# Kernel optimization log

Measured on AMD Instinct MI355X. Metric: run time of the kernel, lower is better.

Reference implementation:

```python
import jax, jax.numpy as jnp
import numpy as np

N, F_IN, E, DIM, G, C = 50000, 128, 800000, 64, 128, 10
BN_EPS = 1e-5


def setup_inputs() -> dict:
    key = jax.random.key(0)
    ks = jax.random.split(key, 24)
    x = jax.random.normal(ks[0], (N, F_IN), dtype=jnp.float32)
    edge_index = jax.random.randint(ks[1], (2, E), 0, N, dtype=jnp.int32)
    batch = jnp.sort(jax.random.randint(ks[2], (N,), 0, G, dtype=jnp.int32))

    def lin(k, fan_in, shape):
        b = 1.0 / np.sqrt(fan_in)
        return jax.random.uniform(k, shape, jnp.float32, -b, b)

    # layer 1 MLP: [F_IN->DIM], [DIM->DIM]
    W1a, b1a = lin(ks[3], F_IN, (F_IN, DIM)), lin(ks[4], F_IN, (DIM,))
    W1b, b1b = lin(ks[5], DIM, (DIM, DIM)), lin(ks[6], DIM, (DIM,))
    # layers 2-5 MLPs stacked: [4, DIM, DIM]
    Wa = jnp.stack([lin(jax.random.fold_in(ks[7], i), DIM, (DIM, DIM)) for i in range(4)])
    ba = jnp.stack([lin(jax.random.fold_in(ks[8], i), DIM, (DIM,)) for i in range(4)])
    Wb = jnp.stack([lin(jax.random.fold_in(ks[9], i), DIM, (DIM, DIM)) for i in range(4)])
    bb = jnp.stack([lin(jax.random.fold_in(ks[10], i), DIM, (DIM,)) for i in range(4)])
    gammas = jnp.ones((5, DIM), jnp.float32)
    betas = jnp.zeros((5, DIM), jnp.float32)
    fc1_w, fc1_b = lin(ks[11], DIM, (DIM, DIM)), lin(ks[12], DIM, (DIM,))
    fc2_w, fc2_b = lin(ks[13], DIM, (DIM, C)), lin(ks[14], DIM, (C,))
    return dict(x=x, edge_index=edge_index, batch=batch,
                W1a=W1a, b1a=b1a, W1b=W1b, b1b=b1b,
                Wa=Wa, ba=ba, Wb=Wb, bb=bb,
                gammas=gammas, betas=betas,
                fc1_w=fc1_w, fc1_b=fc1_b, fc2_w=fc2_w, fc2_b=fc2_b)


def _gin_conv(x, edge_index, W1, b1, W2, b2):
    # PyG GINConv (eps=0): MLP((1+eps)*x + scatter_add of source feats at targets)
    agg = jax.ops.segment_sum(x[edge_index[0]], edge_index[1], num_segments=N)
    h = x + agg
    h = jnp.maximum(h @ W1 + b1, 0.0) @ W2 + b2
    return h


def _bn(h, gamma, beta):
    # BatchNorm1d, training mode (batch statistics, biased variance)
    mean = h.mean(axis=0)
    var = h.var(axis=0)
    return (h - mean) * jax.lax.rsqrt(var + BN_EPS) * gamma + beta


def reference(x, edge_index, batch, W1a, b1a, W1b, b1b, Wa, ba, Wb, bb,
              gammas, betas, fc1_w, fc1_b, fc2_w, fc2_b):
    h = jnp.maximum(_gin_conv(x, edge_index, W1a, b1a, W1b, b1b), 0.0)
    h = _bn(h, gammas[0], betas[0])
    for i in range(4):
        h = jnp.maximum(_gin_conv(h, edge_index, Wa[i], ba[i], Wb[i], bb[i]), 0.0)
        h = _bn(h, gammas[i + 1], betas[i + 1])
    pooled = jax.ops.segment_sum(h, batch, num_segments=G)  # global_add_pool -> [G, DIM]
    z = jnp.maximum(pooled @ fc1_w + fc1_b, 0.0)
    z = z @ fc2_w + fc2_b
    return jax.nn.log_softmax(z, axis=-1)
```

## Files before the change

kernel.cpp:

```cpp
#include <hip/hip_runtime.h>
#include <hip/hip_fp16.h>


constexpr int N = 50000;
constexpr int E = 800000;
constexpr int G = 128;
constexpr int MAXDEG = 64;
constexpr float BN_EPS = 1e-5f;

__device__ inline float4 ld4(const float* p) { return *(const float4*)p; }
__device__ inline void st4(float* p, float4 v) { *(float4*)p = v; }

union HF2 { __half2 h2[2]; float2 f2; };

__global__ __launch_bounds__(256) void count_fill_kernel(
    const int* __restrict__ ei, int* __restrict__ deg, unsigned short* __restrict__ ell)
{
    int e = blockIdx.x * 256 + threadIdx.x;
    if (e < E) {
        int s = ei[e];
        int d = ei[E + e];
        int slot = atomicAdd(&deg[d], 1);
        if (slot < MAXDEG) ell[d * MAXDEG + slot] = (unsigned short)s;
    }
}

__global__ __launch_bounds__(256) void pad_kernel(
    const int* __restrict__ deg, unsigned short* __restrict__ ell)
{
    int n = blockIdx.x * 256 + threadIdx.x;
    if (n < N) {
        int dgc = min(deg[n], MAXDEG);
        int p = (dgc + 7) & ~7;
        for (int s = dgc; s < p; s++) ell[n * MAXDEG + s] = (unsigned short)N;
    }
}

__global__ __launch_bounds__(256) void xw_kernel(
    const float* __restrict__ x, const float* __restrict__ W, __half* __restrict__ out)
{
    int tid = threadIdx.x;
    int ty = tid >> 4, tx = tid & 15;
    int base = blockIdx.x * 64;

    float acc[4][4];
#pragma unroll
    for (int r = 0; r < 4; r++)
#pragma unroll
        for (int cc = 0; cc < 4; cc++) acc[r][cc] = 0.f;

    int rr[4];
#pragma unroll
    for (int r = 0; r < 4; r++) rr[r] = min(base + 4 * ty + r, N - 1);

#pragma unroll 4
    for (int c = 0; c < 128; c++) {
        float4 w4 = ld4(W + c * 64 + 4 * tx);
#pragma unroll
        for (int r = 0; r < 4; r++) {
            float a = x[(size_t)rr[r] * 128 + c];
            acc[r][0] += a * w4.x; acc[r][1] += a * w4.y;
            acc[r][2] += a * w4.z; acc[r][3] += a * w4.w;
        }
    }
#pragma unroll
    for (int r = 0; r < 4; r++) {
        int node = base + 4 * ty + r;
        if (node < N) {
            HF2 u;
            u.h2[0] = __floats2half2_rn(acc[r][0], acc[r][1]);
            u.h2[1] = __floats2half2_rn(acc[r][2], acc[r][3]);
            *(float2*)(out + (size_t)node * 64 + 4 * tx) = u.f2;
        }
    }
}

__global__ __launch_bounds__(64) void reduce_stats_kernel(
    const float* __restrict__ partials, float* __restrict__ stats, int nb)
{
    int c = blockIdx.x;
    int lane = threadIdx.x;
    float s = 0.f;
    for (int i = lane; i < nb; i += 64)
        s += partials[(size_t)i * 128 + c];
#pragma unroll
    for (int off = 32; off > 0; off >>= 1)
        s += __shfl_down(s, off, 64);
    if (lane == 0) stats[c] = s;
}

template <bool FIRST>
__global__ __launch_bounds__(256) void layer_kernel(
    const __half* __restrict__ hin, const unsigned short* __restrict__ ell,
    const int* __restrict__ deg,
    const float* __restrict__ statsPrev, const float* __restrict__ gamma, const float* __restrict__ beta,
    const float* __restrict__ bias0,
    const float* __restrict__ W1, const float* __restrict__ b1,
    const float* __restrict__ W2, const float* __restrict__ b2,
    __half* __restrict__ hout, float* __restrict__ statsPart)
{
    __shared__ float sV[64 * 68];
    __shared__ float sStat[128];

    int tid = threadIdx.x, lane = tid & 63, wv = tid >> 6;
    if (tid < 128) sStat[tid] = 0.f;

    int base = blockIdx.x * 64;
    int n8 = lane >> 3, f = lane & 7;

    float sc[8], sh[8], b0[8];
    if constexpr (FIRST) {
#pragma unroll
        for (int q = 0; q < 2; q++) {
            float4 b4 = ld4(bias0 + 8 * f + 4 * q);
            b0[4 * q + 0] = b4.x; b0[4 * q + 1] = b4.y;
            b0[4 * q + 2] = b4.z; b0[4 * q + 3] = b4.w;
        }
    } else {
#pragma unroll
        for (int q = 0; q < 2; q++) {
            float4 s1 = ld4(statsPrev + 8 * f + 4 * q);
            float4 s2 = ld4(statsPrev + 64 + 8 * f + 4 * q);
            float4 g4 = ld4(gamma + 8 * f + 4 * q);
            float4 be4 = ld4(beta + 8 * f + 4 * q);
            float m[4] = { s1.x / N, s1.y / N, s1.z / N, s1.w / N };
            float v2[4] = { s2.x / N, s2.y / N, s2.z / N, s2.w / N };
            float gg[4] = { g4.x, g4.y, g4.z, g4.w };
            float bb4[4] = { be4.x, be4.y, be4.z, be4.w };
#pragma unroll
            for (int i = 0; i < 4; i++) {
                float s = gg[i] * rsqrtf(v2[i] - m[i] * m[i] + BN_EPS);
                sc[4 * q + i] = s;
                sh[4 * q + i] = bb4[i] - m[i] * s;
            }
        }
    }

#pragma unroll
    for (int kk = 0; kk < 2; kk++) {
        int node = base + wv * 16 + kk * 8 + n8;
        int nd = (node < N) ? node : N;
        int dg = (node < N) ? deg[node] : 0;
        int dgc = min(dg, MAXDEG);
        int p = (dgc + 7) & ~7;
        const unsigned short* row = ell + (size_t)nd * MAXDEG;

        __half2 ap[8][4];
#pragma unroll
        for (int r = 0; r < 8; r++)
#pragma unroll
            for (int k = 0; k < 4; k++) ap[r][k] = __half2(__float2half(0.f), __float2half(0.f));

        float4 rown = ld4((const float*)(hin + (size_t)nd * 64 + 8 * f));

        if (p > 0) {
            uint4 iv = *(const uint4*)(row);
            for (int j = 0; j < p; j += 8) {
                uint4 ivn = iv;
                if (j + 8 < p) ivn = *(const uint4*)(row + j + 8);
                int i0 = iv.x & 0xFFFF, i1 = (int)(iv.x >> 16);
                int i2 = iv.y & 0xFFFF, i3 = (int)(iv.y >> 16);
                int i4 = iv.z & 0xFFFF, i5 = (int)(iv.z >> 16);
                int i6 = iv.w & 0xFFFF, i7 = (int)(iv.w >> 16);
                float4 r0 = ld4((const float*)(hin + (size_t)i0 * 64 + 8 * f));
                float4 r1 = ld4((const float*)(hin + (size_t)i1 * 64 + 8 * f));
                float4 r2 = ld4((const float*)(hin + (size_t)i2 * 64 + 8 * f));
                float4 r3 = ld4((const float*)(hin + (size_t)i3 * 64 + 8 * f));
                float4 r4 = ld4((const float*)(hin + (size_t)i4 * 64 + 8 * f));
                float4 r5 = ld4((const float*)(hin + (size_t)i5 * 64 + 8 * f));
                float4 r6 = ld4((const float*)(hin + (size_t)i6 * 64 + 8 * f));
                float4 r7 = ld4((const float*)(hin + (size_t)i7 * 64 + 8 * f));
                iv = ivn;
                const __half2* h0 = (const __half2*)&r0; const __half2* h1 = (const __half2*)&r1;
                const __half2* h2 = (const __half2*)&r2; const __half2* h3 = (const __half2*)&r3;
                const __half2* h4 = (const __half2*)&r4; const __half2* h5 = (const __half2*)&r5;
                const __half2* h6 = (const __half2*)&r6; const __half2* h7 = (const __half2*)&r7;
#pragma unroll
                for (int k = 0; k < 4; k++) {
                    ap[0][k] = __hadd2(ap[0][k], h0[k]);
                    ap[1][k] = __hadd2(ap[1][k], h1[k]);
                    ap[2][k] = __hadd2(ap[2][k], h2[k]);
                    ap[3][k] = __hadd2(ap[3][k], h3[k]);
                    ap[4][k] = __hadd2(ap[4][k], h4[k]);
                    ap[5][k] = __hadd2(ap[5][k], h5[k]);
                    ap[6][k] = __hadd2(ap[6][k], h6[k]);
                    ap[7][k] = __hadd2(ap[7][k], h7[k]);
                }
            }
        }

        const __half2* ho = (const __half2*)&rown;
        float v[8];
#pragma unroll
        for (int k = 0; k < 4; k++) {
            float2 s = __half22float2(ho[k]);
#pragma unroll
            for (int r = 0; r < 8; r++) {
                float2 fr = __half22float2(ap[r][k]);
                s.x += fr.x; s.y += fr.y;
            }
            if constexpr (FIRST) {
                v[2 * k]     = fmaxf(s.x + b0[2 * k], 0.f);
                v[2 * k + 1] = fmaxf(s.y + b0[2 * k + 1], 0.f);
            } else {
                float dsh = (float)(1 + dg);
                v[2 * k]     = sc[2 * k] * s.x + dsh * sh[2 * k];
                v[2 * k + 1] = sc[2 * k + 1] * s.y + dsh * sh[2 * k + 1];
            }
        }
        int ridx = wv * 16 + kk * 8 + n8;
        st4(sV + ridx * 68 + 8 * f,     make_float4(v[0], v[1], v[2], v[3]));
        st4(sV + ridx * 68 + 8 * f + 4, make_float4(v[4], v[5], v[6], v[7]));
    }
    __syncthreads();

    int ty = tid >> 4, tx = tid & 15;

    if constexpr (!FIRST) {
        float acc[4][4];
#pragma unroll
        for (int cc = 0; cc < 4; cc++) {
            float b = b1[4 * tx + cc];
            acc[0][cc] = b; acc[1][cc] = b; acc[2][cc] = b; acc[3][cc] = b;
        }
#pragma unroll 4
        for (int c = 0; c < 64; c++) {
            float4 w4 = ld4(W1 + c * 64 + 4 * tx);
#pragma unroll
            for (int r = 0; r < 4; r++) {
                float a = sV[(4 * ty + r) * 68 + c];
                acc[r][0] += a * w4.x; acc[r][1] += a * w4.y;
                acc[r][2] += a * w4.z; acc[r][3] += a * w4.w;
            }
        }
        __syncthreads();
#pragma unroll
        for (int r = 0; r < 4; r++)
            st4(sV + (4 * ty + r) * 68 + 4 * tx,
                make_float4(fmaxf(acc[r][0], 0.f), fmaxf(acc[r][1], 0.f),
                            fmaxf(acc[r][2], 0.f), fmaxf(acc[r][3], 0.f)));
        __syncthreads();
    }

    float acc[4][4];
#pragma unroll
    for (int cc = 0; cc < 4; cc++) {
        float b = b2[4 * tx + cc];
        acc[0][cc] = b; acc[1][cc] = b; acc[2][cc] = b; acc[3][cc] = b;
    }
#pragma unroll 4
    for (int c = 0; c < 64; c++) {
        float4 w4 = ld4(W2 + c * 64 + 4 * tx);
#pragma unroll
        for (int r = 0; r < 4; r++) {
            float a = sV[(4 * ty + r) * 68 + c];
            acc[r][0] += a * w4.x; acc[r][1] += a * w4.y;
            acc[r][2] += a * w4.z; acc[r][3] += a * w4.w;
        }
    }
#pragma unroll
    for (int r = 0; r < 4; r++) {
        int node = base + 4 * ty + r;
        if (node < N) {
            acc[r][0] = fmaxf(acc[r][0], 0.f); acc[r][1] = fmaxf(acc[r][1], 0.f);
            acc[r][2] = fmaxf(acc[r][2], 0.f); acc[r][3] = fmaxf(acc[r][3], 0.f);
            HF2 u;
            u.h2[0] = __floats2half2_rn(acc[r][0], acc[r][1]);
            u.h2[1] = __floats2half2_rn(acc[r][2], acc[r][3]);
            *(float2*)(hout + (size_t)node * 64 + 4 * tx) = u.f2;
        } else {
            acc[r][0] = acc[r][1] = acc[r][2] = acc[r][3] = 0.f;
        }
    }
#pragma unroll
    for (int cc = 0; cc < 4; cc++) {
        float s = 0.f, q = 0.f;
#pragma unroll
        for (int r = 0; r < 4; r++) { s += acc[r][cc]; q += acc[r][cc] * acc[r][cc]; }
        atomicAdd(&sStat[4 * tx + cc], s);
        atomicAdd(&sStat[64 + 4 * tx + cc], q);
    }
    __syncthreads();
    if (tid < 128) statsPart[(size_t)blockIdx.x * 128 + tid] = sStat[tid];
}

__global__ __launch_bounds__(256) void pool_head_kernel(
    const __half* __restrict__ h, const int* __restrict__ batch,
    const float* __restrict__ stats, const float* __restrict__ gamma, const float* __restrict__ beta,
    const float* __restrict__ fc1w, const float* __restrict__ fc1b,
    const float* __restrict__ fc2w, const float* __restrict__ fc2b,
    float* __restrict__ out)
{
    __shared__ float sacc[4][64];
    __shared__ float sp[64];
    __shared__ float sz[64];
    __shared__ float so[10];

    int g = blockIdx.x;
    int lane = threadIdx.x & 63, wv = threadIdx.x >> 6;

    int start, end;
    {
        int lo = 0, hi = N;
        while (lo < hi) { int mid = (lo + hi) >> 1; if (batch[mid] < g) lo = mid + 1; else hi = mid; }
        start = lo;
        lo = start; hi = N;
        while (lo < hi) { int mid = (lo + hi) >> 1; if (batch[mid] < g + 1) lo = mid + 1; else hi = mid; }
        end = lo;
    }

    float acc = 0.f;
    for (int node = start + wv; node < end; node += 4)
        acc += __half2float(h[(size_t)node * 64 + lane]);
    sacc[wv][lane] = acc;
    __syncthreads();

    if (wv == 0) {
        float mean = stats[lane] * (1.f / N);
        float var  = stats[64 + lane] * (1.f / N) - mean * mean;
        float sc = gamma[lane] * rsqrtf(var + BN_EPS);
        float sh = beta[lane] - mean * sc;
        float t = sacc[0][lane] + sacc[1][lane] + sacc[2][lane] + sacc[3][lane];
        sp[lane] = sc * t + (float)(end - start) * sh;
    }
    __syncthreads();
    if (wv == 0) {
        float a = fc1b[lane];
#pragma unroll
        for (int c = 0; c < 64; c++) a += sp[c] * fc1w[c * 64 + lane];
        sz[lane] = fmaxf(a, 0.f);
    }
    __syncthreads();
    if (wv == 0 && lane < 10) {
        float z = fc2b[lane];
#pragma unroll
        for (int j = 0; j < 64; j++) z += sz[j] * fc2w[j * 10 + lane];
        so[lane] = z;
    }
    __syncthreads();
    if (wv == 0 && lane < 10) {
        float m = -1e30f;
#pragma unroll
        for (int c = 0; c < 10; c++) m = fmaxf(m, so[c]);
        float s = 0.f;
#pragma unroll
        for (int c = 0; c < 10; c++) s += expf(so[c] - m);
        out[g * 10 + lane] = so[lane] - m - logf(s);
    }
}

extern "C" void kernel_launch(void* const* d_in, const int* in_sizes, int n_in,
                              void* d_out, int out_size, void* d_ws, size_t ws_size,
                              hipStream_t stream)
{
    const float* x    = (const float*)d_in[0];
    const int*   ei   = (const int*)  d_in[1];
    const int*   batch= (const int*)  d_in[2];
    const float* W1a  = (const float*)d_in[3];
    const float* b1a  = (const float*)d_in[4];
    const float* W1b  = (const float*)d_in[5];
    const float* b1b  = (const float*)d_in[6];
    const float* Wa   = (const float*)d_in[7];
    const float* ba   = (const float*)d_in[8];
    const float* Wb   = (const float*)d_in[9];
    const float* bb   = (const float*)d_in[10];
    const float* gammas = (const float*)d_in[11];
    const float* betas  = (const float*)d_in[12];
    const float* fc1w = (const float*)d_in[13];
    const float* fc1b = (const float*)d_in[14];
    const float* fc2w = (const float*)d_in[15];
    const float* fc2b = (const float*)d_in[16];
    float* out = (float*)d_out;

    char* w = (char*)d_ws;
    int*            deg      = (int*)w;
    float*          stats    = (float*)(w + 200704);
    unsigned short* ell      = (unsigned short*)(w + 203264);
    __half*         bufA     = (__half*)(w + 6603264);
    __half*         bufB     = (__half*)(w + 13003392);
    float*          partials = (float*)(w + 19403520);

    hipMemsetAsync(d_ws, 0, 200000, stream);
    hipMemsetAsync(bufA + (size_t)N * 64, 0, 128, stream);
    hipMemsetAsync(bufB + (size_t)N * 64, 0, 128, stream);

    count_fill_kernel<<<(E + 255) / 256, 256, 0, stream>>>(ei, deg, ell);
    pad_kernel<<<(N + 255) / 256, 256, 0, stream>>>(deg, ell);
    xw_kernel<<<(N + 63) / 64, 256, 0, stream>>>(x, W1a, bufA);

    int nb = (N + 63) / 64;

    layer_kernel<true><<<nb, 256, 0, stream>>>(
        bufA, ell, deg, nullptr, nullptr, nullptr, b1a,
        nullptr, nullptr, W1b, b1b, bufB, partials);
    reduce_stats_kernel<<<128, 64, 0, stream>>>(partials, stats, nb);

    layer_kernel<false><<<nb, 256, 0, stream>>>(
        bufB, ell, deg, stats, gammas, betas, nullptr,
        Wa, ba, Wb, bb, bufA, partials);
    reduce_stats_kernel<<<128, 64, 0, stream>>>(partials, stats + 128, nb);

    layer_kernel<false><<<nb, 256, 0, stream>>>(
        bufA, ell, deg, stats + 128, gammas + 64, betas + 64, nullptr,
        Wa + 4096, ba + 64, Wb + 4096, bb + 64, bufB, partials);
    reduce_stats_kernel<<<128, 64, 0, stream>>>(partials, stats + 256, nb);

    layer_kernel<false><<<nb, 256, 0, stream>>>(
        bufB, ell, deg, stats + 256, gammas + 128, betas + 128, nullptr,
        Wa + 8192, ba + 128, Wb + 8192, bb + 128, bufA, partials);
    reduce_stats_kernel<<<128, 64, 0, stream>>>(partials, stats + 384, nb);

    layer_kernel<false><<<nb, 256, 0, stream>>>(
        bufA, ell, deg, stats + 384, gammas + 192, betas + 192, nullptr,
        Wa + 12288, ba + 192, Wb + 12288, bb + 192, bufB, partials);
    reduce_stats_kernel<<<128, 64, 0, stream>>>(partials, stats + 512, nb);

    pool_head_kernel<<<G, 256, 0, stream>>>(
        bufB, batch, stats + 512, gammas + 256, betas + 256,
        fc1w, fc1b, fc2w, fc2b, out);
}
```

Before: 439.6 us.

## Split feature buffers into half-width planes and partition ELL build by destination

Hidden features are stored as two 32-column fp16 planes so each gather pass touches a 3.2MB working set that fits better in cache. The layer kernel now loops over the two planes with 16 nodes per wave instead of 8. The ELL build runs 8 passes, each handling one range of destination nodes, to localize atomics and writes. Padding now comes from memsetting the ELL table to 0xFF and clamping indices to N, which replaces the pad kernel. Outputs and index loads use nontemporal hints. The trade-off is re-reading edge indices eight times in the build and reading each ELL row twice per layer.

```diff
diff --git a/kernel.cpp b/kernel.cpp
--- a/kernel.cpp
+++ b/kernel.cpp
@@ -6,38 +6,36 @@
 constexpr int E = 800000;
 constexpr int G = 128;
 constexpr int MAXDEG = 64;
+constexpr int NPART = 8;
+constexpr int PART_SZ = (N + NPART - 1) / NPART;
 constexpr float BN_EPS = 1e-5f;
+
+typedef unsigned int uintx4 __attribute__((ext_vector_type(4)));
+typedef unsigned int uintx2 __attribute__((ext_vector_type(2)));
 
 __device__ inline float4 ld4(const float* p) { return *(const float4*)p; }
 __device__ inline void st4(float* p, float4 v) { *(float4*)p = v; }
 
-union HF2 { __half2 h2[2]; float2 f2; };
+union HU { __half2 h2[2]; uintx2 u; };
 
 __global__ __launch_bounds__(256) void count_fill_kernel(
     const int* __restrict__ ei, int* __restrict__ deg, unsigned short* __restrict__ ell)
 {
-    int e = blockIdx.x * 256 + threadIdx.x;
+    int part = blockIdx.x & (NPART - 1);
+    int e = (blockIdx.x >> 3) * 256 + threadIdx.x;
     if (e < E) {
-        int s = ei[e];
         int d = ei[E + e];
-        int slot = atomicAdd(&deg[d], 1);
-        if (slot < MAXDEG) ell[d * MAXDEG + slot] = (unsigned short)s;
-    }
-}
-
-__global__ __launch_bounds__(256) void pad_kernel(
-    const int* __restrict__ deg, unsigned short* __restrict__ ell)
-{
-    int n = blockIdx.x * 256 + threadIdx.x;
-    if (n < N) {
-        int dgc = min(deg[n], MAXDEG);
-        int p = (dgc + 7) & ~7;
-        for (int s = dgc; s < p; s++) ell[n * MAXDEG + s] = (unsigned short)N;
+        if (d / PART_SZ == part) {
+            int s = ei[e];
+            int slot = atomicAdd(&deg[d], 1);
+            if (slot < MAXDEG) ell[(size_t)d * MAXDEG + slot] = (unsigned short)s;
+        }
     }
 }
 
 __global__ __launch_bounds__(256) void xw_kernel(
-    const float* __restrict__ x, const float* __restrict__ W, __half* __restrict__ out)
+    const float* __restrict__ x, const float* __restrict__ W,
+    __half* __restrict__ outL, __half* __restrict__ outH)
 {
     int tid = threadIdx.x;
     int ty = tid >> 4, tx = tid & 15;
@@ -67,10 +65,13 @@
     for (int r = 0; r < 4; r++) {
         int node = base + 4 * ty + r;
         if (node < N) {
-            HF2 u;
+            HU u;
             u.h2[0] = __floats2half2_rn(acc[r][0], acc[r][1]);
             u.h2[1] = __floats2half2_rn(acc[r][2], acc[r][3]);
-            *(float2*)(out + (size_t)node * 64 + 4 * tx) = u.f2;
+            if (tx < 8)
+                __builtin_nontemporal_store(u.u, (uintx2*)(outL + (size_t)node * 32 + 4 * tx));
+            else
+                __builtin_nontemporal_store(u.u, (uintx2*)(outH + (size_t)node * 32 + 4 * (tx - 8)));
         }
     }
 }
@@ -91,13 +92,13 @@
 
 template <bool FIRST>
 __global__ __launch_bounds__(256) void layer_kernel(
-    const __half* __restrict__ hin, const unsigned short* __restrict__ ell,
-    const int* __restrict__ deg,
+    const __half* __restrict__ hinL, const __half* __restrict__ hinH,
+    const unsigned short* __restrict__ ell, const int* __restrict__ deg,
     const float* __restrict__ statsPrev, const float* __restrict__ gamma, const float* __restrict__ beta,
     const float* __restrict__ bias0,
     const float* __restrict__ W1, const float* __restrict__ b1,
     const float* __restrict__ W2, const float* __restrict__ b2,
-    __half* __restrict__ hout, float* __restrict__ statsPart)
+    __half* __restrict__ houtL, __half* __restrict__ houtH, float* __restrict__ statsPart)
 {
     __shared__ float sV[64 * 68];
     __shared__ float sStat[128];
@@ -106,90 +107,88 @@
     if (tid < 128) sStat[tid] = 0.f;
 
     int base = blockIdx.x * 64;
-    int n8 = lane >> 3, f = lane & 7;
-
-    float sc[8], sh[8], b0[8];
-    if constexpr (FIRST) {
-#pragma unroll
-        for (int q = 0; q < 2; q++) {
-            float4 b4 = ld4(bias0 + 8 * f + 4 * q);
-            b0[4 * q + 0] = b4.x; b0[4 * q + 1] = b4.y;
-            b0[4 * q + 2] = b4.z; b0[4 * q + 3] = b4.w;
-        }
-    } else {
-#pragma unroll
-        for (int q = 0; q < 2; q++) {
-            float4 s1 = ld4(statsPrev + 8 * f + 4 * q);
-            float4 s2 = ld4(statsPrev + 64 + 8 * f + 4 * q);
-            float4 g4 = ld4(gamma + 8 * f + 4 * q);
-            float4 be4 = ld4(beta + 8 * f + 4 * q);
-            float m[4] = { s1.x / N, s1.y / N, s1.z / N, s1.w / N };
-            float v2[4] = { s2.x / N, s2.y / N, s2.z / N, s2.w / N };
-            float gg[4] = { g4.x, g4.y, g4.z, g4.w };
-            float bb4[4] = { be4.x, be4.y, be4.z, be4.w };
-#pragma unroll
-            for (int i = 0; i < 4; i++) {
-                float s = gg[i] * rsqrtf(v2[i] - m[i] * m[i] + BN_EPS);
-                sc[4 * q + i] = s;
-                sh[4 * q + i] = bb4[i] - m[i] * s;
-            }
-        }
-    }
-
-#pragma unroll
-    for (int kk = 0; kk < 2; kk++) {
-        int node = base + wv * 16 + kk * 8 + n8;
+    int n16 = lane >> 2, f4 = lane & 3;
+
+#pragma unroll
+    for (int P = 0; P < 2; P++) {
+        const __half* hp = P ? hinH : hinL;
+        int c0 = P * 32 + 8 * f4;
+
+        float sc[8], sh[8], b0[8];
+        if constexpr (FIRST) {
+#pragma unroll
+            for (int q = 0; q < 2; q++) {
+                float4 b4 = ld4(bias0 + c0 + 4 * q);
+                b0[4 * q + 0] = b4.x; b0[4 * q + 1] = b4.y;
+                b0[4 * q + 2] = b4.z; b0[4 * q + 3] = b4.w;
+            }
+        } else {
+#pragma unroll
+            for (int q = 0; q < 2; q++) {
+                float4 s1 = ld4(statsPrev + c0 + 4 * q);
+                float4 s2 = ld4(statsPrev + 64 + c0 + 4 * q);
+                float4 g4 = ld4(gamma + c0 + 4 * q);
+                float4 be4 = ld4(beta + c0 + 4 * q);
+                float m[4] = { s1.x / N, s1.y / N, s1.z / N, s1.w / N };
+                float v2[4] = { s2.x / N, s2.y / N, s2.z / N, s2.w / N };
+                float gg[4] = { g4.x, g4.y, g4.z, g4.w };
+                float bb4[4] = { be4.x, be4.y, be4.z, be4.w };
+#pragma unroll
+                for (int i = 0; i < 4; i++) {
+                    float s = gg[i] * rsqrtf(v2[i] - m[i] * m[i] + BN_EPS);
+                    sc[4 * q + i] = s;
+                    sh[4 * q + i] = bb4[i] - m[i] * s;
+                }
+            }
+        }
+
+        int node = base + wv * 16 + n16;
         int nd = (node < N) ? node : N;
         int dg = (node < N) ? deg[node] : 0;
-        int dgc = min(dg, MAXDEG);
-        int p = (dgc + 7) & ~7;
+        int p = (min(dg, MAXDEG) + 7) & ~7;
         const unsigned short* row = ell + (size_t)nd * MAXDEG;
 
         __half2 ap[8][4];
+        __half2 z2 = __half2(__float2half(0.f), __float2half(0.f));
 #pragma unroll
         for (int r = 0; r < 8; r++)
 #pragma unroll
-            for (int k = 0; k < 4; k++) ap[r][k] = __half2(__float2half(0.f), __float2half(0.f));
-
-        float4 rown = ld4((const float*)(hin + (size_t)nd * 64 + 8 * f));
-
-        if (p > 0) {
-            uint4 iv = *(const uint4*)(row);
-            for (int j = 0; j < p; j += 8) {
-                uint4 ivn = iv;
-                if (j + 8 < p) ivn = *(const uint4*)(row + j + 8);
-                int i0 = iv.x & 0xFFFF, i1 = (int)(iv.x >> 16);
-                int i2 = iv.y & 0xFFFF, i3 = (int)(iv.y >> 16);
-                int i4 = iv.z & 0xFFFF, i5 = (int)(iv.z >> 16);
-                int i6 = iv.w & 0xFFFF, i7 = (int)(iv.w >> 16);
-                float4 r0 = ld4((const float*)(hin + (size_t)i0 * 64 + 8 * f));
-                float4 r1 = ld4((const float*)(hin + (size_t)i1 * 64 + 8 * f));
-                float4 r2 = ld4((const float*)(hin + (size_t)i2 * 64 + 8 * f));
-                float4 r3 = ld4((const float*)(hin + (size_t)i3 * 64 + 8 * f));
-                float4 r4 = ld4((const float*)(hin + (size_t)i4 * 64 + 8 * f));
-                float4 r5 = ld4((const float*)(hin + (size_t)i5 * 64 + 8 * f));
-                float4 r6 = ld4((const float*)(hin + (size_t)i6 * 64 + 8 * f));
-                float4 r7 = ld4((const float*)(hin + (size_t)i7 * 64 + 8 * f));
-                iv = ivn;
-                const __half2* h0 = (const __half2*)&r0; const __half2* h1 = (const __half2*)&r1;
-                const __half2* h2 = (const __half2*)&r2; const __half2* h3 = (const __half2*)&r3;
-                const __half2* h4 = (const __half2*)&r4; const __half2* h5 = (const __half2*)&r5;
-                const __half2* h6 = (const __half2*)&r6; const __half2* h7 = (const __half2*)&r7;
-#pragma unroll
-                for (int k = 0; k < 4; k++) {
-                    ap[0][k] = __hadd2(ap[0][k], h0[k]);
-                    ap[1][k] = __hadd2(ap[1][k], h1[k]);
-                    ap[2][k] = __hadd2(ap[2][k], h2[k]);
-                    ap[3][k] = __hadd2(ap[3][k], h3[k]);
-                    ap[4][k] = __hadd2(ap[4][k], h4[k]);
-                    ap[5][k] = __hadd2(ap[5][k], h5[k]);
-                    ap[6][k] = __hadd2(ap[6][k], h6[k]);
-                    ap[7][k] = __hadd2(ap[7][k], h7[k]);
-                }
-            }
-        }
-
-        const __half2* ho = (const __half2*)&rown;
+            for (int k = 0; k < 4; k++) ap[r][k] = z2;
+
+        float4 own = ld4((const float*)(hp + (size_t)nd * 32 + 8 * f4));
+
+        for (int j = 0; j < p; j += 8) {
+            uintx4 iv = __builtin_nontemporal_load((const uintx4*)(row + j));
+            int i0 = min((int)(iv.x & 0xFFFFu), N), i1 = min((int)(iv.x >> 16), N);
+            int i2 = min((int)(iv.y & 0xFFFFu), N), i3 = min((int)(iv.y >> 16), N);
+            int i4 = min((int)(iv.z & 0xFFFFu), N), i5 = min((int)(iv.z >> 16), N);
+            int i6 = min((int)(iv.w & 0xFFFFu), N), i7 = min((int)(iv.w >> 16), N);
+            float4 r0 = ld4((const float*)(hp + (size_t)i0 * 32 + 8 * f4));
+            float4 r1 = ld4((const float*)(hp + (size_t)i1 * 32 + 8 * f4));
+            float4 r2 = ld4((const float*)(hp + (size_t)i2 * 32 + 8 * f4));
+            float4 r3 = ld4((const float*)(hp + (size_t)i3 * 32 + 8 * f4));
+            float4 r4 = ld4((const float*)(hp + (size_t)i4 * 32 + 8 * f4));
+            float4 r5 = ld4((const float*)(hp + (size_t)i5 * 32 + 8 * f4));
+            float4 r6 = ld4((const float*)(hp + (size_t)i6 * 32 + 8 * f4));
+            float4 r7 = ld4((const float*)(hp + (size_t)i7 * 32 + 8 * f4));
+            const __half2* h0 = (const __half2*)&r0; const __half2* h1 = (const __half2*)&r1;
+            const __half2* h2 = (const __half2*)&r2; const __half2* h3 = (const __half2*)&r3;
+            const __half2* h4 = (const __half2*)&r4; const __half2* h5 = (const __half2*)&r5;
+            const __half2* h6 = (const __half2*)&r6; const __half2* h7 = (const __half2*)&r7;
+#pragma unroll
+            for (int k = 0; k < 4; k++) {
+                ap[0][k] = __hadd2(ap[0][k], h0[k]);
+                ap[1][k] = __hadd2(ap[1][k], h1[k]);
+                ap[2][k] = __hadd2(ap[2][k], h2[k]);
+                ap[3][k] = __hadd2(ap[3][k], h3[k]);
+                ap[4][k] = __hadd2(ap[4][k], h4[k]);
+                ap[5][k] = __hadd2(ap[5][k], h5[k]);
+                ap[6][k] = __hadd2(ap[6][k], h6[k]);
+                ap[7][k] = __hadd2(ap[7][k], h7[k]);
+            }
+        }
+
+        const __half2* ho = (const __half2*)&own;
         float v[8];
 #pragma unroll
         for (int k = 0; k < 4; k++) {
@@ -208,9 +207,9 @@
                 v[2 * k + 1] = sc[2 * k + 1] * s.y + dsh * sh[2 * k + 1];
             }
         }
-        int ridx = wv * 16 + kk * 8 + n8;
-        st4(sV + ridx * 68 + 8 * f,     make_float4(v[0], v[1], v[2], v[3]));
-        st4(sV + ridx * 68 + 8 * f + 4, make_float4(v[4], v[5], v[6], v[7]));
+        int nl = wv * 16 + n16;
+        st4(sV + nl * 68 + c0,     make_float4(v[0], v[1], v[2], v[3]));
+        st4(sV + nl * 68 + c0 + 4, make_float4(v[4], v[5], v[6], v[7]));
     }
     __syncthreads();
 
@@ -264,10 +263,13 @@
         if (node < N) {
             acc[r][0] = fmaxf(acc[r][0], 0.f); acc[r][1] = fmaxf(acc[r][1], 0.f);
             acc[r][2] = fmaxf(acc[r][2], 0.f); acc[r][3] = fmaxf(acc[r][3], 0.f);
-            HF2 u;
+            HU u;
             u.h2[0] = __floats2half2_rn(acc[r][0], acc[r][1]);
             u.h2[1] = __floats2half2_rn(acc[r][2], acc[r][3]);
-            *(float2*)(hout + (size_t)node * 64 + 4 * tx) = u.f2;
+            if (tx < 8)
+                __builtin_nontemporal_store(u.u, (uintx2*)(houtL + (size_t)node * 32 + 4 * tx));
+            else
+                __builtin_nontemporal_store(u.u, (uintx2*)(houtH + (size_t)node * 32 + 4 * (tx - 8)));
         } else {
             acc[r][0] = acc[r][1] = acc[r][2] = acc[r][3] = 0.f;
         }
@@ -285,7 +287,7 @@
 }
 
 __global__ __launch_bounds__(256) void pool_head_kernel(
-    const __half* __restrict__ h, const int* __restrict__ batch,
+    const __half* __restrict__ hL, const __half* __restrict__ hH, const int* __restrict__ batch,
     const float* __restrict__ stats, const float* __restrict__ gamma, const float* __restrict__ beta,
     const float* __restrict__ fc1w, const float* __restrict__ fc1b,
     const float* __restrict__ fc2w, const float* __restrict__ fc2b,
@@ -310,8 +312,11 @@
     }
 
     float acc = 0.f;
-    for (int node = start + wv; node < end; node += 4)
-        acc += __half2float(h[(size_t)node * 64 + lane]);
+    for (int node = start + wv; node < end; node += 4) {
+        float hval = (lane < 32) ? __half2float(hL[(size_t)node * 32 + lane])
+                                 : __half2float(hH[(size_t)node * 32 + lane - 32]);
+        acc += hval;
+    }
     sacc[wv][lane] = acc;
     __syncthreads();
 
@@ -376,46 +381,50 @@
     int*            deg      = (int*)w;
     float*          stats    = (float*)(w + 200704);
     unsigned short* ell      = (unsigned short*)(w + 203264);
-    __half*         bufA     = (__half*)(w + 6603264);
-    __half*         bufB     = (__half*)(w + 13003392);
-    float*          partials = (float*)(w + 19403520);
-
-    hipMemsetAsync(d_ws, 0, 200000, stream);
-    hipMemsetAsync(bufA + (size_t)N * 64, 0, 128, stream);
-    hipMemsetAsync(bufB + (size_t)N * 64, 0, 128, stream);
-
-    count_fill_kernel<<<(E + 255) / 256, 256, 0, stream>>>(ei, deg, ell);
-    pad_kernel<<<(N + 255) / 256, 256, 0, stream>>>(deg, ell);
-    xw_kernel<<<(N + 63) / 64, 256, 0, stream>>>(x, W1a, bufA);
+    __half*         bufAL    = (__half*)(w + 6603392);
+    __half*         bufAH    = (__half*)(w + 9803520);
+    __half*         bufBL    = (__half*)(w + 13003648);
+    __half*         bufBH    = (__half*)(w + 16203776);
+    float*          partials = (float*)(w + 19403904);
+
+    hipMemsetAsync(deg, 0, 200000, stream);
+    hipMemsetAsync(ell, 0xFF, 6400128, stream);
+    hipMemsetAsync(bufAL + (size_t)N * 32, 0, 64, stream);
+    hipMemsetAsync(bufAH + (size_t)N * 32, 0, 64, stream);
+    hipMemsetAsync(bufBL + (size_t)N * 32, 0, 64, stream);
+    hipMemsetAsync(bufBH + (size_t)N * 32, 0, 64, stream);
+
+    count_fill_kernel<<<NPART * ((E + 255) / 256), 256, 0, stream>>>(ei, deg, ell);
+    xw_kernel<<<(N + 63) / 64, 256, 0, stream>>>(x, W1a, bufAL, bufAH);
 
     int nb = (N + 63) / 64;
 
     layer_kernel<true><<<nb, 256, 0, stream>>>(
-        bufA, ell, deg, nullptr, nullptr, nullptr, b1a,
-        nullptr, nullptr, W1b, b1b, bufB, partials);
+        bufAL, bufAH, ell, deg, nullptr, nullptr, nullptr, b1a,
+        nullptr, nullptr, W1b, b1b, bufBL, bufBH, partials);
     reduce_stats_kernel<<<128, 64, 0, stream>>>(partials, stats, nb);
 
     layer_kernel<false><<<nb, 256, 0, stream>>>(
-        bufB, ell, deg, stats, gammas, betas, nullptr,
-        Wa, ba, Wb, bb, bufA, partials);
+        bufBL, bufBH, ell, deg, stats, gammas, betas, nullptr,
+        Wa, ba, Wb, bb, bufAL, bufAH, partials);
     reduce_stats_kernel<<<128, 64, 0, stream>>>(partials, stats + 128, nb);
 
     layer_kernel<false><<<nb, 256, 0, stream>>>(
-        bufA, ell, deg, stats + 128, gammas + 64, betas + 64, nullptr,
-        Wa + 4096, ba + 64, Wb + 4096, bb + 64, bufB, partials);
+        bufAL, bufAH, ell, deg, stats + 128, gammas + 64, betas + 64, nullptr,
+        Wa + 4096, ba + 64, Wb + 4096, bb + 64, bufBL, bufBH, partials);
     reduce_stats_kernel<<<128, 64, 0, stream>>>(partials, stats + 256, nb);
 
     layer_kernel<false><<<nb, 256, 0, stream>>>(
-        bufB, ell, deg, stats + 256, gammas + 128, betas + 128, nullptr,
-        Wa + 8192, ba + 128, Wb + 8192, bb + 128, bufA, partials);
+        bufBL, bufBH, ell, deg, stats + 256, gammas + 128, betas + 128, nullptr,
+        Wa + 8192, ba + 128, Wb + 8192, bb + 128, bufAL, bufAH, partials);
     reduce_stats_kernel<<<128, 64, 0, stream>>>(partials, stats + 384, nb);
 
     layer_kernel<false><<<nb, 256, 0, stream>>>(
-        bufA, ell, deg, stats + 384, gammas + 192, betas + 192, nullptr,
-        Wa + 12288, ba + 192, Wb + 12288, bb + 192, bufB, partials);
+        bufAL, bufAH, ell, deg, stats + 384, gammas + 192, betas + 192, nullptr,
+        Wa + 12288, ba + 192, Wb + 12288, bb + 192, bufBL, bufBH, partials);
     reduce_stats_kernel<<<128, 64, 0, stream>>>(partials, stats + 512, nb);
 
     pool_head_kernel<<<G, 256, 0, stream>>>(
-        bufB, batch, stats + 512, gammas + 256, betas + 256,
+        bufBL, bufBH, batch, stats + 512, gammas + 256, betas + 256,
         fc1w, fc1b, fc2w, fc2b, out);
 }
```

After: 493.6 us. +12.3%, slower.
